# Kernel optimization log

Hardware: AMD Instinct MI355X
Metric: run time of the kernel (lower is better)

## Reference

```python
import jax, jax.numpy as jnp
import numpy as np

B, S, VOCAB, P, K, R = 64, 512, 50000, 300, 50, 5


def setup_inputs() -> dict:
    key = jax.random.key(0)
    k0, k1, k2, k3, k4, k5, k6 = jax.random.split(key, 7)
    idx = jax.random.randint(k0, (B, S), 0, VOCAB)
    emb = jax.random.normal(k1, (VOCAB, P), dtype=jnp.float32) * 0.02
    emb = emb.at[0].set(0.0)  # padding_idx=0 row is zero
    C = jax.random.normal(k2, (K, P), dtype=jnp.float32)  # label embeddings ~ N(0,1)
    conv_w = jax.random.normal(k3, (1, 1, 1, 2 * R + 1), dtype=jnp.float32) * 0.1
    conv_b = jax.random.normal(k4, (1,), dtype=jnp.float32) * 0.1
    W2 = jax.random.normal(k5, (K, P), dtype=jnp.float32) / np.sqrt(P).astype(np.float32)
    b2 = jax.random.normal(k6, (K,), dtype=jnp.float32) * 0.01
    return {"idx": idx, "emb": emb, "C": C, "conv_w": conv_w, "conv_b": conv_b, "W2": W2, "b2": b2}


def reference(idx, emb, C, conv_w, conv_b, W2, b2):
    # Embed sentence: [B, S, P]
    x = emb[idx]
    # Cosine label attention
    x_hat = x / (jnp.linalg.norm(x, axis=2, keepdims=True) + 0.001)
    l_hat = C / (jnp.linalg.norm(C, axis=1, keepdims=True) + 0.001)
    G_hat = jnp.einsum('kp,bsp->bks', l_hat, x_hat)  # [B, K, S]
    # Pad seq dim by R on both sides, then conv2d(1->1, kernel (1, 2R+1))
    G_pad = jnp.pad(G_hat, ((0, 0), (0, 0), (R, R)))
    m = jax.lax.conv_general_dilated(
        G_pad[:, None, :, :], conv_w, window_strides=(1, 1), padding='VALID',
        dimension_numbers=('NCHW', 'OIHW', 'NCHW'))[:, 0] + conv_b[0]  # [B, K, S]
    m = jax.nn.relu(m)
    m = jnp.max(m, axis=1)  # max over labels -> [B, S]
    beta = jax.nn.softmax(m, axis=1)[..., None]  # [B, S, 1]
    pooled = jnp.mean(beta * x, axis=1)  # [B, P]
    # Dropout is identity in eval mode; final linear P -> K
    return pooled @ W2.T + b2
```

## Files before the change

kernel.cpp:

```cpp
#include <hip/hip_runtime.h>

#define B_   64
#define S_   512
#define P_   300
#define K_   50
#define MPAD 64
#define LDX  344
#define NS   80
#define LDGS 81

typedef short short8v __attribute__((ext_vector_type(8)));
typedef float float4v __attribute__((ext_vector_type(4)));

__device__ __forceinline__ short f2bf(float f) {
  unsigned u = __builtin_bit_cast(unsigned, f);
  u = (u + 0x7FFFu + ((u >> 16) & 1u)) >> 16;
  return (short)u;
}
__device__ __forceinline__ float bf2f(short h) {
  return __builtin_bit_cast(float, ((unsigned)(unsigned short)h) << 16);
}

__global__ __launch_bounds__(64) void k1_prep(const float* __restrict__ C,
                                              const float* __restrict__ W2,
                                              short* __restrict__ apack) {
  int bid = blockIdx.x;
  int mat = bid / 40;
  int rem = bid - mat * 40;
  int mt  = rem / 10;
  int ks  = rem - mt * 10;
  int lane = threadIdx.x;
  __shared__ float invn[16];
  if (mat == 0) {
    int rl = lane >> 2, q = lane & 3;
    int m = mt * 16 + rl;
    float ss = 0.f;
    if (m < K_) {
      for (int p = q; p < P_; p += 4) { float v = C[m * P_ + p]; ss += v * v; }
    }
    ss += __shfl_xor(ss, 1);
    ss += __shfl_xor(ss, 2);
    if (q == 0) invn[rl] = 1.f / (sqrtf(ss) + 0.001f);
  }
  __syncthreads();
  int ml = lane & 15, quad = lane >> 4;
  int m = mt * 16 + ml;
  const float* src = (mat == 0) ? C : W2;
  short8v v8;
  #pragma unroll
  for (int j = 0; j < 8; ++j) {
    int k = ks * 32 + quad * 8 + j;
    float v = 0.f;
    if (m < K_ && k < P_) {
      v = src[m * P_ + k];
      if (mat == 0) v *= invn[ml];
    }
    v8[j] = f2bf(v);
  }
  *(short8v*)(apack + (size_t)(((mat * 4 + mt) * 10 + ks) * 512 + lane * 8)) = v8;
}

__global__ __launch_bounds__(256) void k2_gemm(const int* __restrict__ idx,
                                               const float* __restrict__ emb,
                                               const short* __restrict__ apack,
                                               short* __restrict__ Yt,
                                               const float* __restrict__ conv_w,
                                               const float* __restrict__ conv_b,
                                               float* __restrict__ mbuf) {
  __shared__ __align__(16) char smem_raw[NS * LDX * 2];
  __shared__ float scale_s[NS];
  __shared__ float mpart[4][64];
  short (*xt)[LDX]  = (short(*)[LDX])smem_raw;
  float (*gs)[LDGS] = (float(*)[LDGS])smem_raw;

  int bid = blockIdx.x;
  int b = bid >> 3, s0 = (bid & 7) * 64;
  int tid = threadIdx.x;
  int w = tid >> 6, lane = tid & 63;

  float ssr[20];
  #pragma unroll
  for (int r = 0; r < 20; ++r) {
    int ls = w * 20 + r;
    int sg = s0 - 8 + ls;
    float ss = 0.f;
    if (sg >= 0 && sg < S_) {
      int row = idx[b * S_ + sg];
      const float4* src = (const float4*)(emb + (size_t)row * P_);
      float4 v = src[lane];
      ss = v.x * v.x + v.y * v.y + v.z * v.z + v.w * v.w;
      short4 h; h.x = f2bf(v.x); h.y = f2bf(v.y); h.z = f2bf(v.z); h.w = f2bf(v.w);
      *(short4*)&xt[ls][4 * lane] = h;
      if (lane < 11) {
        float4 v2 = src[64 + lane];
        ss += v2.x * v2.x + v2.y * v2.y + v2.z * v2.z + v2.w * v2.w;
        short4 h2; h2.x = f2bf(v2.x); h2.y = f2bf(v2.y); h2.z = f2bf(v2.z); h2.w = f2bf(v2.w);
        *(short4*)&xt[ls][256 + 4 * lane] = h2;
      } else if (lane < 16) {
        short4 z = {0, 0, 0, 0};
        *(short4*)&xt[ls][300 + 4 * (lane - 11)] = z;
      }
    } else {
      short4 z = {0, 0, 0, 0};
      *(short4*)&xt[ls][4 * lane] = z;
      if (lane < 11)       *(short4*)&xt[ls][256 + 4 * lane] = z;
      else if (lane < 16)  *(short4*)&xt[ls][300 + 4 * (lane - 11)] = z;
    }
    ssr[r] = ss;
  }
  #pragma unroll
  for (int r = 0; r < 20; ++r) {
    float ss = ssr[r];
    #pragma unroll
    for (int off = 32; off > 0; off >>= 1) ss += __shfl_xor(ss, off);
    if (lane == 0) scale_s[w * 20 + r] = 1.f / (sqrtf(ss) + 0.001f);
  }
  __syncthreads();

  float4v accG[5] = {};
  float4v accY[4] = {};
  int ml = lane & 15, quad = lane >> 4;
  const short8v* a1p = (const short8v*)(apack) + (size_t)((0 * 4 + w) * 10) * 64 + lane;
  const short8v* a2p = (const short8v*)(apack) + (size_t)((1 * 4 + w) * 10) * 64 + lane;
  #pragma unroll
  for (int ks = 0; ks < 10; ++ks) {
    short8v a1 = a1p[ks * 64];
    short8v a2 = a2p[ks * 64];
    int kk = ks * 32 + quad * 8;
    #pragma unroll
    for (int nt = 0; nt < 5; ++nt) {
      short8v bg = *(const short8v*)&xt[nt * 16 + ml][kk];
      accG[nt] = __builtin_amdgcn_mfma_f32_16x16x32_bf16(a1, bg, accG[nt], 0, 0, 0);
    }
    #pragma unroll
    for (int nt = 0; nt < 4; ++nt) {
      short8v by = *(const short8v*)&xt[8 + nt * 16 + ml][kk];
      accY[nt] = __builtin_amdgcn_mfma_f32_16x16x32_bf16(a2, by, accY[nt], 0, 0, 0);
    }
  }

  #pragma unroll
  for (int nt = 0; nt < 4; ++nt) {
    int sg = s0 + nt * 16 + ml;
    #pragma unroll
    for (int reg = 0; reg < 4; ++reg) {
      int m = w * 16 + quad * 4 + reg;
      if (m < K_) Yt[(size_t)(b * MPAD + m) * S_ + sg] = f2bf(accY[nt][reg]);
    }
  }

  float wvv[11];
  #pragma unroll
  for (int t = 0; t < 11; ++t) wvv[t] = conv_w[t];
  float cb = conv_b[0];

  __syncthreads();

  #pragma unroll
  for (int nt = 0; nt < 5; ++nt) {
    int scol = nt * 16 + ml;
    float sc = scale_s[scol];
    #pragma unroll
    for (int reg = 0; reg < 4; ++reg) {
      int m = w * 16 + quad * 4 + reg;
      gs[m][scol] = accG[nt][reg] * sc;
    }
  }
  __syncthreads();

  float part = 0.f;
  for (int k = w; k < K_; k += 4) {
    float acc = cb;
    #pragma unroll
    for (int t = 0; t < 11; ++t) acc += wvv[t] * gs[k][lane + 3 + t];
    part = fmaxf(part, fmaxf(acc, 0.f));
  }
  mpart[w][lane] = part;
  __syncthreads();
  if (tid < 64) {
    float m0 = fmaxf(fmaxf(mpart[0][tid], mpart[1][tid]),
                     fmaxf(mpart[2][tid], mpart[3][tid]));
    mbuf[b * S_ + s0 + tid] = m0;
  }
}

__global__ __launch_bounds__(512) void k3_pool(const float* __restrict__ mbuf,
                                               const short* __restrict__ Yt,
                                               const float* __restrict__ b2,
                                               float* __restrict__ out) {
  __shared__ float beta[S_];
  __shared__ float red[8];
  int b = blockIdx.x;
  int tid = threadIdx.x;
  int lane = tid & 63, wv = tid >> 6;

  float mx = mbuf[b * S_ + tid];

  float r = mx;
  #pragma unroll
  for (int off = 32; off > 0; off >>= 1) r = fmaxf(r, __shfl_xor(r, off));
  if (lane == 0) red[wv] = r;
  __syncthreads();
  float bm = red[0];
  #pragma unroll
  for (int i = 1; i < 8; ++i) bm = fmaxf(bm, red[i]);
  float e = __expf(mx - bm);
  r = e;
  #pragma unroll
  for (int off = 32; off > 0; off >>= 1) r += __shfl_xor(r, off);
  __syncthreads();
  if (lane == 0) red[wv] = r;
  __syncthreads();
  float sum = 0.f;
  #pragma unroll
  for (int i = 0; i < 8; ++i) sum += red[i];
  beta[tid] = e / (sum * (float)S_);
  __syncthreads();

  for (int k = wv; k < K_; k += 8) {
    short8v y = *(const short8v*)(Yt + (((size_t)(b * MPAD + k)) << 9) + lane * 8);
    const float4* bp = (const float4*)&beta[lane * 8];
    float4 b0 = bp[0], b1 = bp[1];
    float acc = b0.x * bf2f(y[0]) + b0.y * bf2f(y[1]) +
                b0.z * bf2f(y[2]) + b0.w * bf2f(y[3]) +
                b1.x * bf2f(y[4]) + b1.y * bf2f(y[5]) +
                b1.z * bf2f(y[6]) + b1.w * bf2f(y[7]);
    #pragma unroll
    for (int off = 32; off > 0; off >>= 1) acc += __shfl_xor(acc, off);
    if (lane == 0) out[b * K_ + k] = acc + b2[k];
  }
}

extern "C" void kernel_launch(void* const* d_in, const int* in_sizes, int n_in,
                              void* d_out, int out_size, void* d_ws, size_t ws_size,
                              hipStream_t stream) {
  const int*   idx    = (const int*)  d_in[0];
  const float* emb    = (const float*)d_in[1];
  const float* C      = (const float*)d_in[2];
  const float* conv_w = (const float*)d_in[3];
  const float* conv_b = (const float*)d_in[4];
  const float* W2     = (const float*)d_in[5];
  const float* b2     = (const float*)d_in[6];
  float* out = (float*)d_out;

  char* ws = (char*)d_ws;
  short* apack = (short*)(ws);
  short* Yt    = (short*)(ws + 81920);
  float* mbuf  = (float*)(ws + 81920 + 4194304);

  hipLaunchKernelGGL(k1_prep, dim3(80),  dim3(64),  0, stream, C, W2, apack);
  hipLaunchKernelGGL(k2_gemm, dim3(512), dim3(256), 0, stream,
                     idx, emb, apack, Yt, conv_w, conv_b, mbuf);
  hipLaunchKernelGGL(k3_pool, dim3(64),  dim3(512), 0, stream, mbuf, Yt, b2, out);
}
```

Baseline: 157.8 us.

## Batch embedding gathers, prefetch A fragments, transpose G scratch layout

The embedding gather is restructured so that all 20 row indices are loaded first and then 10 rows at a time are fetched into registers, instead of one serial index-then-row load per iteration. Out-of-range rows are clamped and zeroed after loading. The packed A fragments are also prefetched into registers before the barrier. The G scratch is transposed with pitch 67 to reduce LDS bank conflicts, and launch bounds request 2 blocks per CU. The aim is more memory-level parallelism on the latency-bound gather, at the cost of higher register pressure.

```diff
diff --git a/kernel.cpp b/kernel.cpp
--- a/kernel.cpp
+++ b/kernel.cpp
@@ -7,7 +7,7 @@
 #define MPAD 64
 #define LDX  344
 #define NS   80
-#define LDGS 81
+#define LDM  67
 
 typedef short short8v __attribute__((ext_vector_type(8)));
 typedef float float4v __attribute__((ext_vector_type(4)));
@@ -60,39 +60,56 @@
   *(short8v*)(apack + (size_t)(((mat * 4 + mt) * 10 + ks) * 512 + lane * 8)) = v8;
 }
 
-__global__ __launch_bounds__(256) void k2_gemm(const int* __restrict__ idx,
-                                               const float* __restrict__ emb,
-                                               const short* __restrict__ apack,
-                                               short* __restrict__ Yt,
-                                               const float* __restrict__ conv_w,
-                                               const float* __restrict__ conv_b,
-                                               float* __restrict__ mbuf) {
+__global__ __launch_bounds__(256, 2) void k2_gemm(const int* __restrict__ idx,
+                                                  const float* __restrict__ emb,
+                                                  const short* __restrict__ apack,
+                                                  short* __restrict__ Yt,
+                                                  const float* __restrict__ conv_w,
+                                                  const float* __restrict__ conv_b,
+                                                  float* __restrict__ mbuf) {
   __shared__ __align__(16) char smem_raw[NS * LDX * 2];
   __shared__ float scale_s[NS];
   __shared__ float mpart[4][64];
-  short (*xt)[LDX]  = (short(*)[LDX])smem_raw;
-  float (*gs)[LDGS] = (float(*)[LDGS])smem_raw;
+  short (*xt)[LDX] = (short(*)[LDX])smem_raw;
+  float (*gst)[LDM] = (float(*)[LDM])smem_raw;
 
   int bid = blockIdx.x;
   int b = bid >> 3, s0 = (bid & 7) * 64;
   int tid = threadIdx.x;
-  int w = tid >> 6, lane = tid & 63;
+  int lane = tid & 63;
+  int wu = __builtin_amdgcn_readfirstlane(tid >> 6);
+
+  int rows[20];
+  #pragma unroll
+  for (int r = 0; r < 20; ++r) {
+    int sg = s0 - 8 + wu * 20 + r;
+    int sgc = sg < 0 ? 0 : (sg >= S_ ? S_ - 1 : sg);
+    rows[r] = idx[b * S_ + sgc];
+  }
 
   float ssr[20];
   #pragma unroll
-  for (int r = 0; r < 20; ++r) {
-    int ls = w * 20 + r;
-    int sg = s0 - 8 + ls;
-    float ss = 0.f;
-    if (sg >= 0 && sg < S_) {
-      int row = idx[b * S_ + sg];
-      const float4* src = (const float4*)(emb + (size_t)row * P_);
-      float4 v = src[lane];
-      ss = v.x * v.x + v.y * v.y + v.z * v.z + v.w * v.w;
-      short4 h; h.x = f2bf(v.x); h.y = f2bf(v.y); h.z = f2bf(v.z); h.w = f2bf(v.w);
-      *(short4*)&xt[ls][4 * lane] = h;
+  for (int h = 0; h < 2; ++h) {
+    float4 va[10], vb[10];
+    #pragma unroll
+    for (int r = 0; r < 10; ++r) {
+      const float4* src = (const float4*)(emb + (size_t)rows[h * 10 + r] * P_);
+      va[r] = src[lane];
+      if (lane < 11) vb[r] = src[64 + lane];
+    }
+    #pragma unroll
+    for (int r = 0; r < 10; ++r) {
+      int ls = wu * 20 + h * 10 + r;
+      int sg = s0 - 8 + ls;
+      bool oob = (sg < 0) || (sg >= S_);
+      float4 v = va[r];
+      if (oob) { v.x = 0.f; v.y = 0.f; v.z = 0.f; v.w = 0.f; }
+      float ss = v.x * v.x + v.y * v.y + v.z * v.z + v.w * v.w;
+      short4 hh; hh.x = f2bf(v.x); hh.y = f2bf(v.y); hh.z = f2bf(v.z); hh.w = f2bf(v.w);
+      *(short4*)&xt[ls][4 * lane] = hh;
       if (lane < 11) {
-        float4 v2 = src[64 + lane];
+        float4 v2 = vb[r];
+        if (oob) { v2.x = 0.f; v2.y = 0.f; v2.z = 0.f; v2.w = 0.f; }
         ss += v2.x * v2.x + v2.y * v2.y + v2.z * v2.z + v2.w * v2.w;
         short4 h2; h2.x = f2bf(v2.x); h2.y = f2bf(v2.y); h2.z = f2bf(v2.z); h2.w = f2bf(v2.w);
         *(short4*)&xt[ls][256 + 4 * lane] = h2;
@@ -100,42 +117,40 @@
         short4 z = {0, 0, 0, 0};
         *(short4*)&xt[ls][300 + 4 * (lane - 11)] = z;
       }
-    } else {
-      short4 z = {0, 0, 0, 0};
-      *(short4*)&xt[ls][4 * lane] = z;
-      if (lane < 11)       *(short4*)&xt[ls][256 + 4 * lane] = z;
-      else if (lane < 16)  *(short4*)&xt[ls][300 + 4 * (lane - 11)] = z;
-    }
-    ssr[r] = ss;
+      ssr[h * 10 + r] = ss;
+    }
   }
   #pragma unroll
   for (int r = 0; r < 20; ++r) {
     float ss = ssr[r];
     #pragma unroll
     for (int off = 32; off > 0; off >>= 1) ss += __shfl_xor(ss, off);
-    if (lane == 0) scale_s[w * 20 + r] = 1.f / (sqrtf(ss) + 0.001f);
-  }
+    if (lane == 0) scale_s[wu * 20 + r] = 1.f / (sqrtf(ss) + 0.001f);
+  }
+
+  const short8v* a1p = (const short8v*)(apack) + (size_t)((0 * 4 + wu) * 10) * 64 + lane;
+  const short8v* a2p = (const short8v*)(apack) + (size_t)((1 * 4 + wu) * 10) * 64 + lane;
+  short8v a1f[10], a2f[10];
+  #pragma unroll
+  for (int ks = 0; ks < 10; ++ks) { a1f[ks] = a1p[ks * 64]; a2f[ks] = a2p[ks * 64]; }
+
   __syncthreads();
 
   float4v accG[5] = {};
   float4v accY[4] = {};
   int ml = lane & 15, quad = lane >> 4;
-  const short8v* a1p = (const short8v*)(apack) + (size_t)((0 * 4 + w) * 10) * 64 + lane;
-  const short8v* a2p = (const short8v*)(apack) + (size_t)((1 * 4 + w) * 10) * 64 + lane;
   #pragma unroll
   for (int ks = 0; ks < 10; ++ks) {
-    short8v a1 = a1p[ks * 64];
-    short8v a2 = a2p[ks * 64];
     int kk = ks * 32 + quad * 8;
     #pragma unroll
     for (int nt = 0; nt < 5; ++nt) {
       short8v bg = *(const short8v*)&xt[nt * 16 + ml][kk];
-      accG[nt] = __builtin_amdgcn_mfma_f32_16x16x32_bf16(a1, bg, accG[nt], 0, 0, 0);
+      accG[nt] = __builtin_amdgcn_mfma_f32_16x16x32_bf16(a1f[ks], bg, accG[nt], 0, 0, 0);
     }
     #pragma unroll
     for (int nt = 0; nt < 4; ++nt) {
       short8v by = *(const short8v*)&xt[8 + nt * 16 + ml][kk];
-      accY[nt] = __builtin_amdgcn_mfma_f32_16x16x32_bf16(a2, by, accY[nt], 0, 0, 0);
+      accY[nt] = __builtin_amdgcn_mfma_f32_16x16x32_bf16(a2f[ks], by, accY[nt], 0, 0, 0);
     }
   }
 
@@ -144,7 +159,7 @@
     int sg = s0 + nt * 16 + ml;
     #pragma unroll
     for (int reg = 0; reg < 4; ++reg) {
-      int m = w * 16 + quad * 4 + reg;
+      int m = wu * 16 + quad * 4 + reg;
       if (m < K_) Yt[(size_t)(b * MPAD + m) * S_ + sg] = f2bf(accY[nt][reg]);
     }
   }
@@ -162,20 +177,20 @@
     float sc = scale_s[scol];
     #pragma unroll
     for (int reg = 0; reg < 4; ++reg) {
-      int m = w * 16 + quad * 4 + reg;
-      gs[m][scol] = accG[nt][reg] * sc;
+      int m = wu * 16 + quad * 4 + reg;
+      gst[scol][m] = accG[nt][reg] * sc;
     }
   }
   __syncthreads();
 
   float part = 0.f;
-  for (int k = w; k < K_; k += 4) {
+  for (int k = wu; k < K_; k += 4) {
     float acc = cb;
     #pragma unroll
-    for (int t = 0; t < 11; ++t) acc += wvv[t] * gs[k][lane + 3 + t];
+    for (int t = 0; t < 11; ++t) acc += wvv[t] * gst[lane + 3 + t][k];
     part = fmaxf(part, fmaxf(acc, 0.f));
   }
-  mpart[w][lane] = part;
+  mpart[wu][lane] = part;
   __syncthreads();
   if (tid < 64) {
     float m0 = fmaxf(fmaxf(mpart[0][tid], mpart[1][tid]),
```

After: 144.9 us. 1.09x faster.
